# Kernel optimization log

Hardware: AMD Instinct MI355X
Metric: run time of the kernel (lower is better)

Reference implementation:

```python
import jax, jax.numpy as jnp
import numpy as np

B, T, D = 1, 2048, 2048
NH, NKV, HD = 16, 4, 128
REP = NH // NKV
ROPE_BASE = 10000.0


def rms_norm(x):
    # matches F.rms_norm default eps = finfo(dtype).eps
    eps = jnp.asarray(jnp.finfo(x.dtype).eps, x.dtype)
    return x * jax.lax.rsqrt(jnp.mean(x * x, axis=-1, keepdims=True) + eps)


def apply_rope(x, cos, sin):
    h = x.shape[-1] // 2
    x1, x2 = x[..., :h], x[..., h:]
    return jnp.concatenate([x1 * cos + x2 * sin, -x1 * sin + x2 * cos], axis=-1)


def setup_inputs() -> dict:
    key = jax.random.key(0)
    ks = jax.random.split(key, 9)
    s = 0.02  # weight init scale
    return {
        "x": jax.random.normal(ks[0], (B, T, D), jnp.float32),
        "skip": jax.random.normal(ks[1], (B, T, D), jnp.float32),
        "wq": jax.random.normal(ks[2], (D, D), jnp.float32) * s,
        "wk": jax.random.normal(ks[3], (NKV * HD, D), jnp.float32) * s,
        "wv": jax.random.normal(ks[4], (NKV * HD, D), jnp.float32) * s,
        "wproj": jax.random.normal(ks[5], (D, D), jnp.float32) * s,
        "qk_g": jnp.ones((NH,), jnp.float32),  # qk_init**0.5 with qk_init=1.0
        "ln_s": jnp.ones((1,), jnp.float32),
        "v_bias": jax.random.normal(ks[6], (NKV, HD), jnp.float32) * 0.01,
    }


def reference(x, skip, wq, wk, wv, wproj, qk_g, ln_s, v_bias):
    Bc, Tc, Dc = x.shape
    q = (x @ wq.T).reshape(Bc, Tc, NH, HD)        # [B,T,NH,HD]
    k = (x @ wk.T).reshape(Bc, Tc, NKV, HD)       # [B,T,NKV,HD]
    v = (x @ wv.T).reshape(Bc, Tc, NKV, HD) + v_bias[None, None, :, :]

    # skip-gate blend
    g = jax.nn.sigmoid(ln_s * 0.1)                # [1]
    ks_ = (skip @ wk.T).reshape(Bc, Tc, NKV, HD)
    vs_ = (skip @ wv.T).reshape(Bc, Tc, NKV, HD)
    k = k * (1.0 - g) + ks_ * g
    v = v * (1.0 - g) + vs_ * g

    q = rms_norm(q)
    k = rms_norm(k)

    # RoPE tables: [1, T, 1, HD/2]
    t = jnp.arange(Tc, dtype=jnp.float32)
    inv_freq = 1.0 / (ROPE_BASE ** (jnp.arange(0, HD, 2, dtype=jnp.float32) / HD))
    fr = t[:, None] * inv_freq[None, :]
    cos = jnp.cos(fr)[None, :, None, :].astype(x.dtype)
    sin = jnp.sin(fr)[None, :, None, :].astype(x.dtype)
    q = apply_rope(q, cos, sin)
    k = apply_rope(k, cos, sin)

    # per-head gain on q and on repeated k (effective gain^2 on logits)
    gain = jnp.abs(qk_g).astype(x.dtype)          # [NH]
    q = q * gain[None, None, :, None]
    k = jnp.repeat(k, REP, axis=2) * gain[None, None, :, None]  # [B,T,NH,HD]
    v = jnp.repeat(v, REP, axis=2)                               # [B,T,NH,HD]

    scale = 1.0 / jnp.sqrt(jnp.asarray(HD, x.dtype))
    scores = jnp.einsum('bqhd,bkhd->bhqk', q, k) * scale         # [B,NH,T,T]
    causal = jnp.tril(jnp.ones((Tc, Tc), dtype=bool))
    scores = jnp.where(causal[None, None], scores, -jnp.inf)
    attn = jax.nn.softmax(scores, axis=-1)
    y = jnp.einsum('bhqk,bkhd->bqhd', attn, v).reshape(Bc, Tc, Dc)
    return (y @ wproj.T) * ln_s.astype(x.dtype)
```

## Files before the change

### kernel.cpp

```cpp
#include <hip/hip_runtime.h>


typedef float  f32x4 __attribute__((ext_vector_type(4)));
typedef short  s16x8 __attribute__((ext_vector_type(8)));
typedef unsigned short u16;

#define DEVI __device__ __forceinline__

DEVI u16 f2bf(float f) {
  union { float f; unsigned u; } c; c.f = f;
  unsigned u = c.u + 0x7fffu + ((c.u >> 16) & 1u);
  return (u16)(u >> 16);
}

DEVI void gl_lds16(const void* g, void* l) {
  __builtin_amdgcn_global_load_lds(
      (const __attribute__((address_space(1))) unsigned int*)g,
      (__attribute__((address_space(3))) unsigned int*)l, 16, 0, 0);
}

__global__ __launch_bounds__(256) void prep_kernel(
    const float* __restrict__ x, const float* __restrict__ skip,
    const float* __restrict__ ln_s, const float* __restrict__ v_bias,
    const float* __restrict__ qk_g, u16* __restrict__ xb, u16* __restrict__ xmb,
    float* __restrict__ colbias, float* __restrict__ hscale) {
  float g = 1.0f / (1.0f + __expf(-ln_s[0] * 0.1f));
  int i = (blockIdx.x * 256 + threadIdx.x) * 4;
  float4 xv = *(const float4*)(x + i);
  float4 sv = *(const float4*)(skip + i);
  ushort4 a, b;
  a.x = f2bf(xv.x); a.y = f2bf(xv.y); a.z = f2bf(xv.z); a.w = f2bf(xv.w);
  b.x = f2bf((1.f - g) * xv.x + g * sv.x);
  b.y = f2bf((1.f - g) * xv.y + g * sv.y);
  b.z = f2bf((1.f - g) * xv.z + g * sv.z);
  b.w = f2bf((1.f - g) * xv.w + g * sv.w);
  *(ushort4*)(xb + i) = a;
  *(ushort4*)(xmb + i) = b;
  if (blockIdx.x == 0) {
    int t = threadIdx.x;
    for (int k = t; k < 512; k += 256) {
      colbias[k] = 0.f;
      colbias[512 + k] = (1.f - g) * v_bias[k];
    }
    if (t < 16) { float gq = qk_g[t]; hscale[t] = gq * gq * 0.08838834764831845f; }
  }
}

__global__ __launch_bounds__(256) void convw_kernel(
    const float* __restrict__ wq, const float* __restrict__ wk,
    const float* __restrict__ wv, const float* __restrict__ wp,
    u16* __restrict__ wb) {
  size_t i = ((size_t)blockIdx.x * 256 + threadIdx.x) * 4;
  constexpr size_t M4 = 4u * 1024 * 1024, M1 = 1024 * 1024;
  const float* src;
  if (i < M4) src = wq + i;
  else if (i < M4 + M1) src = wk + (i - M4);
  else if (i < M4 + 2 * M1) src = wv + (i - M4 - M1);
  else src = wp + (i - M4 - 2 * M1);
  float4 v = *(const float4*)src;
  ushort4 o;
  o.x = f2bf(v.x); o.y = f2bf(v.y); o.z = f2bf(v.z); o.w = f2bf(v.w);
  *(ushort4*)(wb + i) = o;
}

template <int BIAS, int SCALE>
__global__ __launch_bounds__(256) void gemm_nt(
    const u16* __restrict__ A, const u16* __restrict__ B, float* __restrict__ C,
    int M, int N, int K, const float* __restrict__ bias,
    const float* __restrict__ scale) {
  __shared__ u16 lA[128 * 32];
  __shared__ u16 lB[128 * 32];
  const int tid = threadIdx.x;
  const int lane = tid & 63, w = tid >> 6;
  const int m0 = blockIdx.y * 128, n0 = blockIdx.x * 128;
  const int mo = (w >> 1) * 64, no = (w & 1) * 64;
  const int r16 = lane & 15, q4 = lane >> 4;
  f32x4 acc[4][4] = {};

  for (int k0 = 0; k0 < K; k0 += 32) {
#pragma unroll
    for (int j = 0; j < 2; ++j) {
      int slot = j * 256 + tid;
      int row = slot >> 2, c8 = (slot & 3) * 8;
      gl_lds16(A + (size_t)(m0 + row) * K + k0 + c8, &lA[slot * 8]);
    }
#pragma unroll
    for (int j = 0; j < 2; ++j) {
      int slot = j * 256 + tid;
      int row = slot >> 2, c8 = (slot & 3) * 8;
      gl_lds16(B + (size_t)(n0 + row) * K + k0 + c8, &lB[slot * 8]);
    }
    __syncthreads();
    s16x8 af[4], bfr[4];
#pragma unroll
    for (int i = 0; i < 4; ++i)
      af[i] = *(const s16x8*)&lA[(mo + i * 16 + r16) * 32 + q4 * 8];
#pragma unroll
    for (int i = 0; i < 4; ++i)
      bfr[i] = *(const s16x8*)&lB[(no + i * 16 + r16) * 32 + q4 * 8];
#pragma unroll
    for (int mi = 0; mi < 4; ++mi)
#pragma unroll
      for (int ni = 0; ni < 4; ++ni)
        acc[mi][ni] = __builtin_amdgcn_mfma_f32_16x16x32_bf16(
            af[mi], bfr[ni], acc[mi][ni], 0, 0, 0);
    __syncthreads();
  }
  float sc = SCALE ? scale[0] : 1.0f;
#pragma unroll
  for (int mi = 0; mi < 4; ++mi) {
#pragma unroll
    for (int ni = 0; ni < 4; ++ni) {
      int col = n0 + no + ni * 16 + r16;
      float bv = BIAS ? bias[col] : 0.0f;
#pragma unroll
      for (int r = 0; r < 4; ++r) {
        int row = m0 + mo + mi * 16 + q4 * 4 + r;
        C[(size_t)row * N + col] = (acc[mi][ni][r] + bv) * sc;
      }
    }
  }
}

__global__ __launch_bounds__(256) void postqk_kernel(
    const float* __restrict__ qraw, const float* __restrict__ kvraw,
    u16* __restrict__ qb, u16* __restrict__ kb) {
  constexpr int T = 2048;
  const int lane = threadIdx.x & 63, w = threadIdx.x >> 6;
  int p = blockIdx.x * 4 + w;
  const float* src;
  u16* dst;
  int t;
  if (p < 16 * T) {
    int hh = p >> 11; t = p & 2047;
    src = qraw + (size_t)t * 2048 + hh * 128;
    dst = qb + ((size_t)hh * T + t) * 128;
  } else {
    p -= 16 * T;
    int hh = p >> 11; t = p & 2047;
    src = kvraw + (size_t)t * 1024 + hh * 128;
    dst = kb + ((size_t)hh * T + t) * 128;
  }
  float x1 = src[lane], x2 = src[lane + 64];
  float ss = x1 * x1 + x2 * x2;
  ss += __shfl_xor(ss, 1);  ss += __shfl_xor(ss, 2);  ss += __shfl_xor(ss, 4);
  ss += __shfl_xor(ss, 8);  ss += __shfl_xor(ss, 16); ss += __shfl_xor(ss, 32);
  float rn = rsqrtf(ss * (1.0f / 128.0f) + 1.1920929e-7f);
  float fr = (float)t * expf((float)lane * -0.14391156831212787f);
  float c = cosf(fr), s = sinf(fr);
  float y1 = (x1 * c + x2 * s) * rn;
  float y2 = (x2 * c - x1 * s) * rn;
  dst[lane] = f2bf(y1);
  dst[lane + 64] = f2bf(y2);
}

__global__ __launch_bounds__(256) void transv_kernel(
    const float* __restrict__ kvraw, u16* __restrict__ vT) {
  constexpr int T = 2048;
  __shared__ float tile[32][33];
  int t0 = blockIdx.x * 32, hd0 = blockIdx.y * 32;
  int tx = threadIdx.x & 31, ty = threadIdx.x >> 5;
#pragma unroll
  for (int i = 0; i < 4; ++i) {
    int t = t0 + ty + i * 8;
    tile[ty + i * 8][tx] = kvraw[(size_t)t * 1024 + 512 + hd0 + tx];
  }
  __syncthreads();
#pragma unroll
  for (int i = 0; i < 4; ++i) {
    int hd = hd0 + ty + i * 8;
    vT[(size_t)hd * T + t0 + tx] = f2bf(tile[tx][ty + i * 8]);
  }
}

__global__ __launch_bounds__(256) void flash_kernel(
    const u16* __restrict__ qb, const u16* __restrict__ kb,
    const u16* __restrict__ vT, u16* __restrict__ out,
    const float* __restrict__ hscale) {
  constexpr int T = 2048;
  __shared__ u16 lK[32 * 128];
  __shared__ u16 lV[128 * 32];
  __shared__ u16 lP[4][16 * 56];
  const int tid = threadIdx.x, lane = tid & 63, w = tid >> 6;
  const int h = blockIdx.y, hkv = h >> 2;
  const int q0 = (int)(gridDim.x - 1 - blockIdx.x) * 64;
  const int r16 = lane & 15, q4 = lane >> 4;

  s16x8 qf[4];
  {
    const u16* qp = qb + ((size_t)h * T + q0 + w * 16 + r16) * 128 + q4 * 8;
#pragma unroll
    for (int d = 0; d < 4; ++d) qf[d] = *(const s16x8*)(qp + d * 32);
  }
  const float sc = hscale[h];
  f32x4 O[8] = {};
  float m_[4], l_[4];
#pragma unroll
  for (int r = 0; r < 4; ++r) { m_[r] = -3.0e38f; l_[r] = 0.f; }
  const int qrow = q0 + w * 16 + q4 * 4;
  const int nt = (q0 + 64) / 32;

  for (int it = 0; it < nt; ++it) {
    const int t0 = it * 32;
#pragma unroll
    for (int j = 0; j < 2; ++j) {
      int slot = j * 256 + tid;
      int row = slot >> 4;
      int cb = ((slot & 15) * 16) ^ ((row & 7) << 4);
      gl_lds16(kb + ((size_t)hkv * T + t0 + row) * 128 + (cb >> 1), &lK[slot * 8]);
    }
#pragma unroll
    for (int j = 0; j < 2; ++j) {
      int slot = j * 256 + tid;
      int row = slot >> 2;
      int cb = ((slot & 3) * 16) ^ (((row >> 1) & 3) << 4);
      gl_lds16(vT + ((size_t)hkv * 128 + row) * T + t0 + (cb >> 1), &lV[slot * 8]);
    }
    __syncthreads();

    f32x4 s0 = {}, s1 = {};
#pragma unroll
    for (int d = 0; d < 4; ++d) {
      int cb = (q4 * 16 + d * 64) ^ ((r16 & 7) << 4);
      s16x8 kf = *(const s16x8*)&lK[r16 * 128 + (cb >> 1)];
      s0 = __builtin_amdgcn_mfma_f32_16x16x32_bf16(qf[d], kf, s0, 0, 0, 0);
    }
#pragma unroll
    for (int d = 0; d < 4; ++d) {
      int krow = 16 + r16;
      int cb = (q4 * 16 + d * 64) ^ ((krow & 7) << 4);
      s16x8 kf = *(const s16x8*)&lK[krow * 128 + (cb >> 1)];
      s1 = __builtin_amdgcn_mfma_f32_16x16x32_bf16(qf[d], kf, s1, 0, 0, 0);
    }
    float sv0[4], sv1[4];
#pragma unroll
    for (int r = 0; r < 4; ++r) {
      sv0[r] = (t0 + r16      <= qrow + r) ? s0[r] * sc : -3.0e38f;
      sv1[r] = (t0 + 16 + r16 <= qrow + r) ? s1[r] * sc : -3.0e38f;
    }
    float al[4];
#pragma unroll
    for (int r = 0; r < 4; ++r) {
      float t = fmaxf(sv0[r], sv1[r]);
      t = fmaxf(t, __shfl_xor(t, 1));
      t = fmaxf(t, __shfl_xor(t, 2));
      t = fmaxf(t, __shfl_xor(t, 4));
      t = fmaxf(t, __shfl_xor(t, 8));
      float mn = fmaxf(m_[r], t);
      al[r] = __expf(m_[r] - mn);
      m_[r] = mn;
    }
    u16* myP = &lP[w][0];
#pragma unroll
    for (int r = 0; r < 4; ++r) {
      float p0 = __expf(sv0[r] - m_[r]);
      float p1 = __expf(sv1[r] - m_[r]);
      int row = q4 * 4 + r;
      myP[row * 56 + r16] = f2bf(p0);
      myP[row * 56 + 16 + r16] = f2bf(p1);
      float s = p0 + p1;
      s += __shfl_xor(s, 1); s += __shfl_xor(s, 2);
      s += __shfl_xor(s, 4); s += __shfl_xor(s, 8);
      l_[r] = l_[r] * al[r] + s;
    }
#pragma unroll
    for (int dt = 0; dt < 8; ++dt)
#pragma unroll
      for (int r = 0; r < 4; ++r) O[dt][r] *= al[r];
    asm volatile("s_waitcnt lgkmcnt(0)" ::: "memory");
    s16x8 pf = *(const s16x8*)&myP[r16 * 56 + q4 * 8];
#pragma unroll
    for (int dt = 0; dt < 8; ++dt) {
      int vrow = dt * 16 + r16;
      int cb = (q4 * 16) ^ (((vrow >> 1) & 3) << 4);
      s16x8 vf = *(const s16x8*)&lV[vrow * 32 + (cb >> 1)];
      O[dt] = __builtin_amdgcn_mfma_f32_16x16x32_bf16(pf, vf, O[dt], 0, 0, 0);
    }
    __syncthreads();
  }
  float inv[4];
#pragma unroll
  for (int r = 0; r < 4; ++r) inv[r] = 1.0f / l_[r];
#pragma unroll
  for (int dt = 0; dt < 8; ++dt) {
#pragma unroll
    for (int r = 0; r < 4; ++r) {
      int row = qrow + r;
      int col = h * 128 + dt * 16 + r16;
      out[(size_t)row * 2048 + col] = f2bf(O[dt][r] * inv[r]);
    }
  }
}

extern "C" void kernel_launch(void* const* d_in, const int* in_sizes, int n_in,
                              void* d_out, int out_size, void* d_ws,
                              size_t ws_size, hipStream_t stream) {
  const float* x      = (const float*)d_in[0];
  const float* skip   = (const float*)d_in[1];
  const float* wq     = (const float*)d_in[2];
  const float* wk     = (const float*)d_in[3];
  const float* wv     = (const float*)d_in[4];
  const float* wp     = (const float*)d_in[5];
  const float* qk_g   = (const float*)d_in[6];
  const float* ln_s   = (const float*)d_in[7];
  const float* v_bias = (const float*)d_in[8];
  float* out = (float*)d_out;

  constexpr size_t MB = 1024 * 1024;
  char* ws = (char*)d_ws;
  u16*   wb    = (u16*)(ws);
  u16*   xb    = (u16*)(ws + 20 * MB);
  u16*   xmb   = (u16*)(ws + 28 * MB);
  float* qraw  = (float*)(ws + 36 * MB);
  float* kvraw = (float*)(ws + 52 * MB);
  u16*   qb    = (u16*)(ws + 60 * MB);
  u16*   kb    = (u16*)(ws + 68 * MB);
  u16*   vT    = (u16*)(ws + 70 * MB);
  u16*   ao    = (u16*)(ws + 72 * MB);
  float* colbias = (float*)(ws + 80 * MB);
  float* hscale  = (float*)(ws + 80 * MB + 4096);

  prep_kernel<<<4096, 256, 0, stream>>>(x, skip, ln_s, v_bias, qk_g, xb, xmb,
                                        colbias, hscale);
  convw_kernel<<<10240, 256, 0, stream>>>(wq, wk, wv, wp, wb);
  gemm_nt<0, 0><<<dim3(16, 16), 256, 0, stream>>>(xb, wb, qraw, 2048, 2048,
                                                  2048, nullptr, nullptr);
  gemm_nt<1, 0><<<dim3(8, 16), 256, 0, stream>>>(
      xmb, wb + 4 * MB, kvraw, 2048, 1024, 2048, colbias, nullptr);
  postqk_kernel<<<10240, 256, 0, stream>>>(qraw, kvraw, qb, kb);
  transv_kernel<<<dim3(64, 16), 256, 0, stream>>>(kvraw, vT);
  flash_kernel<<<dim3(32, 16), 256, 0, stream>>>(qb, kb, vT, ao, hscale);
  gemm_nt<0, 1><<<dim3(16, 16), 256, 0, stream>>>(
      ao, wb + 6 * MB, out, 2048, 2048, 2048, nullptr, ln_s);
}
```

Measured before the change: 403.5 us.

## Double-buffer K/V tiles in flash attention with 64-key blocks and exp2 softmax

The flash kernel now processes 64 keys per iteration instead of 32 and double-buffers the K and V tiles in LDS, prefetching the next tile while the current one is computed. This should hide global-load latency and halve the number of barriers. The softmax scale and log2(e) are folded into the q normalization in postqk, so the kernel can use exp2 directly. The causal mask is applied only on diagonal tiles. LDS use grows, which may lower occupancy.

```diff
diff --git a/kernel.cpp b/kernel.cpp
--- a/kernel.cpp
+++ b/kernel.cpp
@@ -22,8 +22,7 @@
 __global__ __launch_bounds__(256) void prep_kernel(
     const float* __restrict__ x, const float* __restrict__ skip,
     const float* __restrict__ ln_s, const float* __restrict__ v_bias,
-    const float* __restrict__ qk_g, u16* __restrict__ xb, u16* __restrict__ xmb,
-    float* __restrict__ colbias, float* __restrict__ hscale) {
+    u16* __restrict__ xb, u16* __restrict__ xmb, float* __restrict__ colbias) {
   float g = 1.0f / (1.0f + __expf(-ln_s[0] * 0.1f));
   int i = (blockIdx.x * 256 + threadIdx.x) * 4;
   float4 xv = *(const float4*)(x + i);
@@ -42,7 +41,6 @@
       colbias[k] = 0.f;
       colbias[512 + k] = (1.f - g) * v_bias[k];
     }
-    if (t < 16) { float gq = qk_g[t]; hscale[t] = gq * gq * 0.08838834764831845f; }
   }
 }
 
@@ -124,17 +122,21 @@
 
 __global__ __launch_bounds__(256) void postqk_kernel(
     const float* __restrict__ qraw, const float* __restrict__ kvraw,
-    u16* __restrict__ qb, u16* __restrict__ kb) {
+    const float* __restrict__ qk_g, u16* __restrict__ qb,
+    u16* __restrict__ kb) {
   constexpr int T = 2048;
   const int lane = threadIdx.x & 63, w = threadIdx.x >> 6;
   int p = blockIdx.x * 4 + w;
   const float* src;
   u16* dst;
   int t;
+  float extra = 1.0f;
   if (p < 16 * T) {
     int hh = p >> 11; t = p & 2047;
     src = qraw + (size_t)t * 2048 + hh * 128;
     dst = qb + ((size_t)hh * T + t) * 128;
+    float g = qk_g[hh];
+    extra = g * g * 0.12751742f;
   } else {
     p -= 16 * T;
     int hh = p >> 11; t = p & 2047;
@@ -145,7 +147,7 @@
   float ss = x1 * x1 + x2 * x2;
   ss += __shfl_xor(ss, 1);  ss += __shfl_xor(ss, 2);  ss += __shfl_xor(ss, 4);
   ss += __shfl_xor(ss, 8);  ss += __shfl_xor(ss, 16); ss += __shfl_xor(ss, 32);
-  float rn = rsqrtf(ss * (1.0f / 128.0f) + 1.1920929e-7f);
+  float rn = rsqrtf(ss * (1.0f / 128.0f) + 1.1920929e-7f) * extra;
   float fr = (float)t * expf((float)lane * -0.14391156831212787f);
   float c = cosf(fr), s = sinf(fr);
   float y1 = (x1 * c + x2 * s) * rn;
@@ -175,16 +177,16 @@
 
 __global__ __launch_bounds__(256) void flash_kernel(
     const u16* __restrict__ qb, const u16* __restrict__ kb,
-    const u16* __restrict__ vT, u16* __restrict__ out,
-    const float* __restrict__ hscale) {
+    const u16* __restrict__ vT, u16* __restrict__ out) {
   constexpr int T = 2048;
-  __shared__ u16 lK[32 * 128];
-  __shared__ u16 lV[128 * 32];
-  __shared__ u16 lP[4][16 * 56];
+  __shared__ u16 lK[2][64 * 128];
+  __shared__ u16 lV[2][128 * 64];
+  __shared__ u16 lP[4][16 * 72];
   const int tid = threadIdx.x, lane = tid & 63, w = tid >> 6;
   const int h = blockIdx.y, hkv = h >> 2;
   const int q0 = (int)(gridDim.x - 1 - blockIdx.x) * 64;
   const int r16 = lane & 15, q4 = lane >> 4;
+  const int qrow = q0 + w * 16 + q4 * 4;
 
   s16x8 qf[4];
   {
@@ -192,92 +194,126 @@
 #pragma unroll
     for (int d = 0; d < 4; ++d) qf[d] = *(const s16x8*)(qp + d * 32);
   }
-  const float sc = hscale[h];
+
+  const u16* kbase = kb + (size_t)hkv * T * 128;
+  const u16* vbase = vT + (size_t)hkv * 128 * T;
+  int ks_off[4], vs_off[4];
+#pragma unroll
+  for (int j = 0; j < 4; ++j) {
+    int slot = j * 256 + tid;
+    int krow = slot >> 4, kc = slot & 15;
+    int kcb = (kc * 16) ^ ((krow & 7) << 4);
+    ks_off[j] = krow * 128 + (kcb >> 1);
+    int vrow = slot >> 3, vc = slot & 7;
+    int vcb = (vc * 16) ^ ((vrow & 7) << 4);
+    vs_off[j] = vrow * T + (vcb >> 1);
+  }
+
   f32x4 O[8] = {};
   float m_[4], l_[4];
 #pragma unroll
   for (int r = 0; r < 4; ++r) { m_[r] = -3.0e38f; l_[r] = 0.f; }
-  const int qrow = q0 + w * 16 + q4 * 4;
-  const int nt = (q0 + 64) / 32;
+  const int nt = q0 / 64 + 1;
+
+#pragma unroll
+  for (int j = 0; j < 4; ++j)
+    gl_lds16(kbase + ks_off[j], &lK[0][(j * 256 + tid) * 8]);
+#pragma unroll
+  for (int j = 0; j < 4; ++j)
+    gl_lds16(vbase + vs_off[j], &lV[0][(j * 256 + tid) * 8]);
+  asm volatile("s_waitcnt vmcnt(0)" ::: "memory");
+  __builtin_amdgcn_s_barrier();
 
   for (int it = 0; it < nt; ++it) {
-    const int t0 = it * 32;
-#pragma unroll
-    for (int j = 0; j < 2; ++j) {
-      int slot = j * 256 + tid;
-      int row = slot >> 4;
-      int cb = ((slot & 15) * 16) ^ ((row & 7) << 4);
-      gl_lds16(kb + ((size_t)hkv * T + t0 + row) * 128 + (cb >> 1), &lK[slot * 8]);
-    }
-#pragma unroll
-    for (int j = 0; j < 2; ++j) {
-      int slot = j * 256 + tid;
-      int row = slot >> 2;
-      int cb = ((slot & 3) * 16) ^ (((row >> 1) & 3) << 4);
-      gl_lds16(vT + ((size_t)hkv * 128 + row) * T + t0 + (cb >> 1), &lV[slot * 8]);
-    }
-    __syncthreads();
-
-    f32x4 s0 = {}, s1 = {};
-#pragma unroll
-    for (int d = 0; d < 4; ++d) {
-      int cb = (q4 * 16 + d * 64) ^ ((r16 & 7) << 4);
-      s16x8 kf = *(const s16x8*)&lK[r16 * 128 + (cb >> 1)];
-      s0 = __builtin_amdgcn_mfma_f32_16x16x32_bf16(qf[d], kf, s0, 0, 0, 0);
-    }
-#pragma unroll
-    for (int d = 0; d < 4; ++d) {
-      int krow = 16 + r16;
-      int cb = (q4 * 16 + d * 64) ^ ((krow & 7) << 4);
-      s16x8 kf = *(const s16x8*)&lK[krow * 128 + (cb >> 1)];
-      s1 = __builtin_amdgcn_mfma_f32_16x16x32_bf16(qf[d], kf, s1, 0, 0, 0);
-    }
-    float sv0[4], sv1[4];
+    const int t0 = it * 64;
+    const int cur = it & 1;
+    if (it + 1 < nt) {
+      const int nxt = (it + 1) * 64;
+#pragma unroll
+      for (int j = 0; j < 4; ++j)
+        gl_lds16(kbase + (size_t)nxt * 128 + ks_off[j],
+                 &lK[cur ^ 1][(j * 256 + tid) * 8]);
+#pragma unroll
+      for (int j = 0; j < 4; ++j)
+        gl_lds16(vbase + nxt + vs_off[j],
+                 &lV[cur ^ 1][(j * 256 + tid) * 8]);
+    }
+    const u16* Kt = lK[cur];
+    const u16* Vt = lV[cur];
+
+    f32x4 s[4];
+#pragma unroll
+    for (int kvh = 0; kvh < 4; ++kvh) {
+      f32x4 acc = {};
+#pragma unroll
+      for (int d = 0; d < 4; ++d) {
+        int cb = ((q4 * 16 + d * 64) ^ ((r16 & 7) << 4)) >> 1;
+        acc = __builtin_amdgcn_mfma_f32_16x16x32_bf16(
+            qf[d], *(const s16x8*)(Kt + (kvh * 16 + r16) * 128 + cb), acc, 0, 0, 0);
+      }
+      s[kvh] = acc;
+    }
+
+    if (t0 + 64 > q0 + w * 16) {
+#pragma unroll
+      for (int kvh = 0; kvh < 4; ++kvh)
+#pragma unroll
+        for (int r = 0; r < 4; ++r)
+          s[kvh][r] = (t0 + kvh * 16 + r16 <= qrow + r) ? s[kvh][r] : -1.0e30f;
+    }
+
+    float al[4];
 #pragma unroll
     for (int r = 0; r < 4; ++r) {
-      sv0[r] = (t0 + r16      <= qrow + r) ? s0[r] * sc : -3.0e38f;
-      sv1[r] = (t0 + 16 + r16 <= qrow + r) ? s1[r] * sc : -3.0e38f;
-    }
-    float al[4];
-#pragma unroll
-    for (int r = 0; r < 4; ++r) {
-      float t = fmaxf(sv0[r], sv1[r]);
+      float t = fmaxf(fmaxf(s[0][r], s[1][r]), fmaxf(s[2][r], s[3][r]));
       t = fmaxf(t, __shfl_xor(t, 1));
       t = fmaxf(t, __shfl_xor(t, 2));
       t = fmaxf(t, __shfl_xor(t, 4));
       t = fmaxf(t, __shfl_xor(t, 8));
       float mn = fmaxf(m_[r], t);
-      al[r] = __expf(m_[r] - mn);
+      al[r] = __builtin_amdgcn_exp2f(m_[r] - mn);
       m_[r] = mn;
     }
-    u16* myP = &lP[w][0];
+    u16* myP = lP[w];
 #pragma unroll
     for (int r = 0; r < 4; ++r) {
-      float p0 = __expf(sv0[r] - m_[r]);
-      float p1 = __expf(sv1[r] - m_[r]);
-      int row = q4 * 4 + r;
-      myP[row * 56 + r16] = f2bf(p0);
-      myP[row * 56 + 16 + r16] = f2bf(p1);
-      float s = p0 + p1;
-      s += __shfl_xor(s, 1); s += __shfl_xor(s, 2);
-      s += __shfl_xor(s, 4); s += __shfl_xor(s, 8);
-      l_[r] = l_[r] * al[r] + s;
+      float ps = 0.f;
+      int prow = (q4 * 4 + r) * 72;
+#pragma unroll
+      for (int kvh = 0; kvh < 4; ++kvh) {
+        float pp = __builtin_amdgcn_exp2f(s[kvh][r] - m_[r]);
+        myP[prow + kvh * 16 + r16] = f2bf(pp);
+        ps += pp;
+      }
+      ps += __shfl_xor(ps, 1); ps += __shfl_xor(ps, 2);
+      ps += __shfl_xor(ps, 4); ps += __shfl_xor(ps, 8);
+      l_[r] = l_[r] * al[r] + ps;
     }
 #pragma unroll
     for (int dt = 0; dt < 8; ++dt)
 #pragma unroll
       for (int r = 0; r < 4; ++r) O[dt][r] *= al[r];
+
     asm volatile("s_waitcnt lgkmcnt(0)" ::: "memory");
-    s16x8 pf = *(const s16x8*)&myP[r16 * 56 + q4 * 8];
+    __builtin_amdgcn_sched_barrier(0);
+    s16x8 pf0 = *(const s16x8*)&myP[r16 * 72 + q4 * 8];
+    s16x8 pf1 = *(const s16x8*)&myP[r16 * 72 + 32 + q4 * 8];
+
+    int cb0 = ((q4 * 16) ^ ((r16 & 7) << 4)) >> 1;
+    int cb1 = ((64 + q4 * 16) ^ ((r16 & 7) << 4)) >> 1;
 #pragma unroll
     for (int dt = 0; dt < 8; ++dt) {
-      int vrow = dt * 16 + r16;
-      int cb = (q4 * 16) ^ (((vrow >> 1) & 3) << 4);
-      s16x8 vf = *(const s16x8*)&lV[vrow * 32 + (cb >> 1)];
-      O[dt] = __builtin_amdgcn_mfma_f32_16x16x32_bf16(pf, vf, O[dt], 0, 0, 0);
-    }
-    __syncthreads();
-  }
+      const u16* vr = Vt + (dt * 16 + r16) * 64;
+      O[dt] = __builtin_amdgcn_mfma_f32_16x16x32_bf16(
+          pf0, *(const s16x8*)(vr + cb0), O[dt], 0, 0, 0);
+      O[dt] = __builtin_amdgcn_mfma_f32_16x16x32_bf16(
+          pf1, *(const s16x8*)(vr + cb1), O[dt], 0, 0, 0);
+    }
+
+    asm volatile("s_waitcnt vmcnt(0)" ::: "memory");
+    __builtin_amdgcn_s_barrier();
+  }
+
   float inv[4];
 #pragma unroll
   for (int r = 0; r < 4; ++r) inv[r] = 1.0f / l_[r];
@@ -318,18 +354,17 @@
   u16*   vT    = (u16*)(ws + 70 * MB);
   u16*   ao    = (u16*)(ws + 72 * MB);
   float* colbias = (float*)(ws + 80 * MB);
-  float* hscale  = (float*)(ws + 80 * MB + 4096);
-
-  prep_kernel<<<4096, 256, 0, stream>>>(x, skip, ln_s, v_bias, qk_g, xb, xmb,
-                                        colbias, hscale);
+
+  prep_kernel<<<4096, 256, 0, stream>>>(x, skip, ln_s, v_bias, xb, xmb,
+                                        colbias);
   convw_kernel<<<10240, 256, 0, stream>>>(wq, wk, wv, wp, wb);
   gemm_nt<0, 0><<<dim3(16, 16), 256, 0, stream>>>(xb, wb, qraw, 2048, 2048,
                                                   2048, nullptr, nullptr);
   gemm_nt<1, 0><<<dim3(8, 16), 256, 0, stream>>>(
       xmb, wb + 4 * MB, kvraw, 2048, 1024, 2048, colbias, nullptr);
-  postqk_kernel<<<10240, 256, 0, stream>>>(qraw, kvraw, qb, kb);
+  postqk_kernel<<<10240, 256, 0, stream>>>(qraw, kvraw, qk_g, qb, kb);
   transv_kernel<<<dim3(64, 16), 256, 0, stream>>>(kvraw, vT);
-  flash_kernel<<<dim3(32, 16), 256, 0, stream>>>(qb, kb, vT, ao, hscale);
+  flash_kernel<<<dim3(32, 16), 256, 0, stream>>>(qb, kb, vT, ao);
   gemm_nt<0, 1><<<dim3(16, 16), 256, 0, stream>>>(
       ao, wb + 6 * MB, out, 2048, 2048, 2048, nullptr, ln_s);
 }
```

New measurement: 354.7 us. 1.14x faster.
